# Optimization experiments

Hardware: AMD Instinct MI355X
Metric: run time of the kernel (lower is better)

Reference implementation:

```python
import jax, jax.numpy as jnp
import numpy as np

N = 100000      # num vertices
M = 100000      # num hyperedges
NNZ = 800000    # incidence pairs
IN_CH = 128
H, C = 8, 16    # heads, out_channels
NEG_SLOPE = 0.2


def setup_inputs() -> dict:
    key = jax.random.key(0)
    k1, k2, k3, k4, k5 = jax.random.split(key, 5)
    X = jax.random.normal(k1, (N, IN_CH), dtype=jnp.float32)
    vertex = jax.random.randint(k2, (NNZ,), 0, N, dtype=jnp.int32)
    edges = jax.random.randint(k3, (NNZ,), 0, M, dtype=jnp.int32)
    # glorot init: Linear W (in, H*C) and att_e (1, H, C)
    std_w = float(np.sqrt(6.0 / (IN_CH + H * C)))
    W = jax.random.uniform(k4, (IN_CH, H * C), minval=-std_w, maxval=std_w, dtype=jnp.float32)
    std_a = float(np.sqrt(6.0 / (H + C)))
    att_e = jax.random.uniform(k5, (1, H, C), minval=-std_a, maxval=std_a, dtype=jnp.float32)
    return {"X": X, "W": W, "att_e": att_e, "vertex": vertex, "edges": edges}


def reference(X, W, att_e, vertex, edges):
    Nn = X.shape[0]
    nnz = vertex.shape[0]
    # X0 = self.W(X)  -> (N, H*C), then view (N, H, C)
    X0 = X @ W
    Xh = X0.reshape(Nn, H, C)
    # gather per incidence, mean-aggregate to hyperedges (first_aggregate='mean')
    Xve = Xh[vertex]                                            # (nnz, H, C)
    e_sum = jax.ops.segment_sum(Xve, edges, num_segments=M)     # (M, H, C)
    e_cnt = jax.ops.segment_sum(jnp.ones((nnz,), X.dtype), edges, num_segments=M)
    Xe = e_sum / jnp.maximum(e_cnt, 1.0)[:, None, None]
    # edge attention logits
    alpha_e = (Xe * att_e).sum(-1)                              # (M, H)
    a = alpha_e[edges]                                          # (nnz, H)
    a = jnp.where(a >= 0, a, NEG_SLOPE * a)                     # leaky_relu
    # segment softmax over incidences grouped by destination vertex
    amax = jax.ops.segment_max(a, vertex, num_segments=Nn)      # (N, H)
    amax = jnp.where(jnp.isfinite(amax), amax, 0.0)
    ex = jnp.exp(a - amax[vertex])
    denom = jax.ops.segment_sum(ex, vertex, num_segments=Nn)
    alpha = ex / (denom[vertex] + 1e-16)                        # (nnz, H)
    # attention-weighted scatter-sum back to vertices
    Xev = Xe[edges] * alpha[:, :, None]                         # (nnz, H, C)
    Xv = jax.ops.segment_sum(Xev, vertex, num_segments=Nn)      # (N, H, C)
    return Xv.reshape(Nn, H * C)
```

## Files before the change

kernel.cpp:

```cpp
#include <hip/hip_runtime.h>
#include <hip/hip_bf16.h>

#define N_V   100000
#define N_E   100000
#define NNZ_C 800000
#define HC    128
#define H_    8
#define C_    16
#define NEG   0.2f
#define BSH   9
#define KPB   512
#define NBUCK 196
#define CAP   5120
#define CHUNK 4096
#define SCAT_NB ((NNZ_C + CHUNK - 1) / CHUNK)
#define GEMM_NB ((N_V + 63) / 64)

typedef __attribute__((ext_vector_type(8))) short bf16x8;
typedef __attribute__((ext_vector_type(4))) float f32x4;
typedef unsigned long long ull;

__device__ __forceinline__ short f2bf(float f) {
    unsigned u = __float_as_uint(f);
    unsigned r = (u + 0x7FFFu + ((u >> 16) & 1u)) >> 16;
    return (short)r;
}
__device__ __forceinline__ float bf2f(unsigned short u) {
    return __uint_as_float(((unsigned)u) << 16);
}
__device__ __forceinline__ unsigned pack2(float lo, float hi) {
    return ((unsigned)(unsigned short)f2bf(hi) << 16) | (unsigned short)f2bf(lo);
}
__device__ __forceinline__ void acc8w(float* acc, uint4 p, float wt) {
    acc[0] += __uint_as_float(p.x << 16) * wt;
    acc[1] += __uint_as_float(p.x & 0xFFFF0000u) * wt;
    acc[2] += __uint_as_float(p.y << 16) * wt;
    acc[3] += __uint_as_float(p.y & 0xFFFF0000u) * wt;
    acc[4] += __uint_as_float(p.z << 16) * wt;
    acc[5] += __uint_as_float(p.z & 0xFFFF0000u) * wt;
    acc[6] += __uint_as_float(p.w << 16) * wt;
    acc[7] += __uint_as_float(p.w & 0xFFFF0000u) * wt;
}
__device__ __forceinline__ void acc8(float* acc, uint4 p) {
    acc[0] += __uint_as_float(p.x << 16);
    acc[1] += __uint_as_float(p.x & 0xFFFF0000u);
    acc[2] += __uint_as_float(p.y << 16);
    acc[3] += __uint_as_float(p.y & 0xFFFF0000u);
    acc[4] += __uint_as_float(p.z << 16);
    acc[5] += __uint_as_float(p.z & 0xFFFF0000u);
    acc[6] += __uint_as_float(p.w << 16);
    acc[7] += __uint_as_float(p.w & 0xFFFF0000u);
}

__global__ __launch_bounds__(256) void wt_k(const float* __restrict__ W, unsigned short* __restrict__ Wf) {
    int i = blockIdx.x * 256 + threadIdx.x;
    int j    = i & 7;
    int lane = (i >> 3) & 63;
    int ct   = (i >> 9) & 7;
    int ks   = i >> 12;
    int kq = lane >> 4, cl = lane & 15;
    int k = 32 * ks + ((j < 4) ? (4 * kq + j) : (16 + 4 * kq + (j - 4)));
    int c = 16 * ct + cl;
    Wf[i] = (unsigned short)f2bf(W[k * 128 + c]);
}

__global__ __launch_bounds__(256) void fusedA_k(const float* __restrict__ X,
                                                const unsigned short* __restrict__ Wf,
                                                unsigned short* __restrict__ X0b,
                                                const int* __restrict__ edges,
                                                const int* __restrict__ vertex,
                                                int* __restrict__ bcur_e, int* __restrict__ bcur_v,
                                                unsigned* __restrict__ stage_e, unsigned* __restrict__ stage_v) {
    __shared__ int he[NBUCK], hv[NBUCK];
    int tid = threadIdx.x;

    if (blockIdx.x >= SCAT_NB) {
        int blk = blockIdx.x - SCAT_NB;
        int lane = tid & 63;
        int cl = lane & 15, kq = lane >> 4;
        int base = blk * 64 + (tid >> 6) * 16;
        int rowA = base + cl;
        int srcRow = (rowA < N_V) ? rowA : (N_V - 1);

        f32x4 acc[8] = {};
        const float4* X4 = (const float4*)X;
        const bf16x8* Wf8 = (const bf16x8*)Wf;

        #pragma unroll
        for (int ks = 0; ks < 4; ++ks) {
            float4 a0 = X4[(size_t)srcRow * 32 + 8 * ks + kq];
            float4 a1 = X4[(size_t)srcRow * 32 + 8 * ks + 4 + kq];
            bf16x8 af;
            af[0] = f2bf(a0.x); af[1] = f2bf(a0.y); af[2] = f2bf(a0.z); af[3] = f2bf(a0.w);
            af[4] = f2bf(a1.x); af[5] = f2bf(a1.y); af[6] = f2bf(a1.z); af[7] = f2bf(a1.w);
            #pragma unroll
            for (int ct = 0; ct < 8; ++ct) {
                bf16x8 bf = Wf8[((ks * 8 + ct) << 6) + lane];
                acc[ct] = __builtin_amdgcn_mfma_f32_16x16x32_bf16(af, bf, acc[ct], 0, 0, 0);
            }
        }
        int rbase = base + kq * 4;
        #pragma unroll
        for (int ct = 0; ct < 8; ++ct) {
            #pragma unroll
            for (int r = 0; r < 4; ++r) {
                int row = rbase + r;
                if (row < N_V) X0b[(size_t)row * 128 + ct * 16 + cl] = (unsigned short)f2bf(acc[ct][r]);
            }
        }
    } else {
        for (int i = tid; i < NBUCK; i += 256) { he[i] = 0; hv[i] = 0; }
        __syncthreads();
        int e0 = blockIdx.x * CHUNK;
        int e1 = e0 + CHUNK; if (e1 > NNZ_C) e1 = NNZ_C;
        for (int i = e0 + tid; i < e1; i += 256) {
            atomicAdd(&he[edges[i] >> BSH], 1);
            atomicAdd(&hv[vertex[i] >> BSH], 1);
        }
        __syncthreads();
        for (int i = tid; i < NBUCK; i += 256) {
            int c = he[i]; he[i] = c ? atomicAdd(&bcur_e[i], c) : 0;
            c = hv[i];     hv[i] = c ? atomicAdd(&bcur_v[i], c) : 0;
        }
        __syncthreads();
        for (int i = e0 + tid; i < e1; i += 256) {
            int ed = edges[i], v = vertex[i];
            int be = ed >> BSH, bv = v >> BSH;
            int pe = atomicAdd(&he[be], 1);
            stage_e[(size_t)be * CAP + pe] = ((unsigned)(ed & (KPB - 1)) << 17) | (unsigned)v;
            int pv = atomicAdd(&hv[bv], 1);
            stage_v[(size_t)bv * CAP + pv] = ((unsigned)(v & (KPB - 1)) << 17) | (unsigned)ed;
        }
    }
}

__global__ __launch_bounds__(512) void bsort_k(const unsigned* __restrict__ stage_e,
                                               const unsigned* __restrict__ stage_v,
                                               const int* __restrict__ bcur_e, const int* __restrict__ bcur_v,
                                               int* __restrict__ e_off, int* __restrict__ v_off,
                                               int* __restrict__ e_idx, int* __restrict__ v_idx) {
    bool isE = blockIdx.x < NBUCK;
    int b = isE ? blockIdx.x : blockIdx.x - NBUCK;
    const unsigned* stage = (isE ? stage_e : stage_v) + (size_t)b * CAP;
    const int* bcnt = isE ? bcur_e : bcur_v;
    int* off = isE ? e_off : v_off;
    int* idx = isE ? e_idx : v_idx;
    int t = threadIdx.x;

    __shared__ int sb[256];
    __shared__ int cntk[KPB];
    __shared__ int loc[KPB];
    if (t < 256) sb[t] = (t < NBUCK) ? bcnt[t] : 0;
    cntk[t] = 0;
    __syncthreads();
    for (int dd = 1; dd < 256; dd <<= 1) {
        int v = (t < 256 && t >= dd) ? sb[t - dd] : 0;
        __syncthreads();
        if (t < 256 && t >= dd) sb[t] += v;
        __syncthreads();
    }
    int cnt = bcnt[b];
    int bbase = sb[b] - cnt;

    for (int i = t; i < cnt; i += 512)
        atomicAdd(&cntk[stage[i] >> 17], 1);
    __syncthreads();
    int val = cntk[t];
    loc[t] = val;
    __syncthreads();
    for (int dd = 1; dd < 512; dd <<= 1) {
        int tv = (t >= dd) ? loc[t - dd] : 0;
        __syncthreads();
        loc[t] += tv;
        __syncthreads();
    }
    int pos0 = bbase + loc[t] - val;
    int key = (b << BSH) + t;
    if (key < N_V) off[key] = pos0;
    cntk[t] = pos0;
    __syncthreads();
    for (int i = t; i < cnt; i += 512) {
        unsigned p = stage[i];
        int pos = atomicAdd(&cntk[p >> 17], 1);
        idx[pos] = (int)(p & 0x1FFFF);
    }
    if (blockIdx.x == 0 && t == 0) { e_off[N_E] = NNZ_C; v_off[N_V] = NNZ_C; }
}

__global__ __launch_bounds__(256) void agg_gather_k(const uint4* __restrict__ X0b4,
                                                    const int* __restrict__ e_off,
                                                    const int* __restrict__ e_idx,
                                                    const float* __restrict__ att,
                                                    uint4* __restrict__ Xeb4,
                                                    float* __restrict__ alpha_l) {
    int wave = (int)((blockIdx.x * 256 + threadIdx.x) >> 6);
    int lane = threadIdx.x & 63;
    if (wave >= N_E) return;
    int beg = e_off[wave], end = e_off[wave + 1];
    int deg = end - beg;
    int j = lane & 15, g = lane >> 4;

    float acc[8] = {0.f, 0.f, 0.f, 0.f, 0.f, 0.f, 0.f, 0.f};
    const uint4 Z = {0u, 0u, 0u, 0u};

    if (deg <= 64) {
        int vl = (lane < deg) ? e_idx[beg + lane] : 0;
        for (int r0 = 0; r0 < deg; r0 += 16) {
            int r_0 = r0 + g, r_1 = r0 + 4 + g, r_2 = r0 + 8 + g, r_3 = r0 + 12 + g;
            int v_0 = __shfl(vl, r_0), v_1 = __shfl(vl, r_1);
            int v_2 = __shfl(vl, r_2), v_3 = __shfl(vl, r_3);
            uint4 p_0 = Z, p_1 = Z, p_2 = Z, p_3 = Z;
            if (r_0 < deg) p_0 = X0b4[(size_t)v_0 * 16 + j];
            if (r_1 < deg) p_1 = X0b4[(size_t)v_1 * 16 + j];
            if (r_2 < deg) p_2 = X0b4[(size_t)v_2 * 16 + j];
            if (r_3 < deg) p_3 = X0b4[(size_t)v_3 * 16 + j];
            acc8(acc, p_0); acc8(acc, p_1); acc8(acc, p_2); acc8(acc, p_3);
        }
    } else {
        for (int i0 = beg; i0 < end; i0 += 4) {
            int i = i0 + g;
            uint4 p = Z;
            if (i < end) p = X0b4[(size_t)e_idx[i] * 16 + j];
            acc8(acc, p);
        }
    }
    #pragma unroll
    for (int k = 0; k < 8; ++k) {
        acc[k] += __shfl_xor(acc[k], 16);
        acc[k] += __shfl_xor(acc[k], 32);
    }
    float inv = 1.f / fmaxf((float)deg, 1.f);
    uint4 o;
    o.x = pack2(acc[0] * inv, acc[1] * inv);
    o.y = pack2(acc[2] * inv, acc[3] * inv);
    o.z = pack2(acc[4] * inv, acc[5] * inv);
    o.w = pack2(acc[6] * inv, acc[7] * inv);
    if (g == 0) Xeb4[(size_t)wave * 16 + j] = o;

    const float4* att4 = (const float4*)att;
    float4 A0 = att4[2 * j], A1 = att4[2 * j + 1];
    float s = bf2f((unsigned short)(o.x & 0xFFFF)) * A0.x + bf2f((unsigned short)(o.x >> 16)) * A0.y
            + bf2f((unsigned short)(o.y & 0xFFFF)) * A0.z + bf2f((unsigned short)(o.y >> 16)) * A0.w
            + bf2f((unsigned short)(o.z & 0xFFFF)) * A1.x + bf2f((unsigned short)(o.z >> 16)) * A1.y
            + bf2f((unsigned short)(o.w & 0xFFFF)) * A1.z + bf2f((unsigned short)(o.w >> 16)) * A1.w;
    s += __shfl_xor(s, 1);
    if (g == 0 && (j & 1) == 0) {
        s = (s >= 0.f) ? s : NEG * s;
        alpha_l[wave * 8 + (j >> 1)] = s;
    }
}

__global__ __launch_bounds__(256) void out_fused_k(const uint4* __restrict__ Xeb4,
                                                   const float* __restrict__ alpha_l,
                                                   const int* __restrict__ v_off,
                                                   const int* __restrict__ v_idx,
                                                   float* __restrict__ out) {
    int wave = (int)((blockIdx.x * 256 + threadIdx.x) >> 6);
    int lane = threadIdx.x & 63;
    if (wave >= N_V) return;
    int beg = v_off[wave], end = v_off[wave + 1];
    int deg = end - beg;
    int j = lane & 15, g = lane >> 4, h = j >> 1;

    float acc[8] = {0.f, 0.f, 0.f, 0.f, 0.f, 0.f, 0.f, 0.f};
    float d = 0.f;
    const uint4 Z = {0u, 0u, 0u, 0u};

    if (deg <= 64) {
        int vl = (lane < deg) ? v_idx[beg + lane] : 0;
        for (int r0 = 0; r0 < deg; r0 += 16) {
            int r_0 = r0 + g, r_1 = r0 + 4 + g, r_2 = r0 + 8 + g, r_3 = r0 + 12 + g;
            int e_0 = __shfl(vl, r_0), e_1 = __shfl(vl, r_1);
            int e_2 = __shfl(vl, r_2), e_3 = __shfl(vl, r_3);
            bool b_0 = r_0 < deg, b_1 = r_1 < deg, b_2 = r_2 < deg, b_3 = r_3 < deg;
            float a_0 = 0.f, a_1 = 0.f, a_2 = 0.f, a_3 = 0.f;
            uint4 p_0 = Z, p_1 = Z, p_2 = Z, p_3 = Z;
            if (b_0) { a_0 = alpha_l[e_0 * 8 + h]; p_0 = Xeb4[(size_t)e_0 * 16 + j]; }
            if (b_1) { a_1 = alpha_l[e_1 * 8 + h]; p_1 = Xeb4[(size_t)e_1 * 16 + j]; }
            if (b_2) { a_2 = alpha_l[e_2 * 8 + h]; p_2 = Xeb4[(size_t)e_2 * 16 + j]; }
            if (b_3) { a_3 = alpha_l[e_3 * 8 + h]; p_3 = Xeb4[(size_t)e_3 * 16 + j]; }
            float w_0 = b_0 ? __expf(a_0) : 0.f;
            float w_1 = b_1 ? __expf(a_1) : 0.f;
            float w_2 = b_2 ? __expf(a_2) : 0.f;
            float w_3 = b_3 ? __expf(a_3) : 0.f;
            d += w_0 + w_1 + w_2 + w_3;
            acc8w(acc, p_0, w_0); acc8w(acc, p_1, w_1);
            acc8w(acc, p_2, w_2); acc8w(acc, p_3, w_3);
        }
    } else {
        for (int i0 = beg; i0 < end; i0 += 4) {
            int i = i0 + g;
            float w = 0.f;
            uint4 p = Z;
            if (i < end) {
                int ed = v_idx[i];
                w = __expf(alpha_l[ed * 8 + h]);
                p = Xeb4[(size_t)ed * 16 + j];
            }
            d += w;
            acc8w(acc, p, w);
        }
    }
    d += __shfl_xor(d, 16);
    d += __shfl_xor(d, 32);
    float rd = 1.f / (d + 1e-16f);
    #pragma unroll
    for (int k = 0; k < 8; ++k) {
        acc[k] += __shfl_xor(acc[k], 16);
        acc[k] += __shfl_xor(acc[k], 32);
        acc[k] *= rd;
    }
    if (g == 0) {
        float4* out4 = (float4*)out;
        float4 o0 = {acc[0], acc[1], acc[2], acc[3]};
        float4 o1 = {acc[4], acc[5], acc[6], acc[7]};
        out4[(size_t)wave * 32 + 2 * j]     = o0;
        out4[(size_t)wave * 32 + 2 * j + 1] = o1;
    }
}

extern "C" void kernel_launch(void* const* d_in, const int* in_sizes, int n_in,
                              void* d_out, int out_size, void* d_ws, size_t ws_size,
                              hipStream_t stream) {
    const float* X      = (const float*)d_in[0];
    const float* W      = (const float*)d_in[1];
    const float* att    = (const float*)d_in[2];
    const int*   vertex = (const int*)d_in[3];
    const int*   edges  = (const int*)d_in[4];
    float* out = (float*)d_out;

    unsigned short* X0b = (unsigned short*)d_ws;
    unsigned short* Xeb = X0b + (size_t)N_V * HC;
    unsigned* stage_e = (unsigned*)(Xeb + (size_t)N_E * HC);
    unsigned* stage_v = stage_e + (size_t)NBUCK * CAP;
    int*   e_off   = (int*)(stage_v + (size_t)NBUCK * CAP);
    int*   v_off   = e_off + (N_E + 1);
    int*   e_idx   = v_off + (N_V + 1);
    int*   v_idx   = e_idx + NNZ_C;
    float* alpha_l = (float*)(v_idx + NNZ_C);
    int*   bcur_e  = (int*)(alpha_l + (size_t)N_E * H_);
    int*   bcur_v  = bcur_e + NBUCK;
    unsigned short* Wf = (unsigned short*)(bcur_v + NBUCK);

    hipMemsetAsync(bcur_e, 0, sizeof(int) * 2 * NBUCK, stream);

    wt_k<<<64, 256, 0, stream>>>(W, Wf);

    fusedA_k<<<SCAT_NB + GEMM_NB, 256, 0, stream>>>(X, Wf, X0b, edges, vertex,
                                                    bcur_e, bcur_v, stage_e, stage_v);

    bsort_k<<<2 * NBUCK, 512, 0, stream>>>(stage_e, stage_v, bcur_e, bcur_v,
                                           e_off, v_off, e_idx, v_idx);

    agg_gather_k<<<(N_E * 64) / 256, 256, 0, stream>>>((const uint4*)X0b, e_off, e_idx, att,
                                                       (uint4*)Xeb, alpha_l);

    out_fused_k<<<(N_V * 64) / 256, 256, 0, stream>>>((const uint4*)Xeb, alpha_l, v_off, v_idx, out);
}
```

Baseline: 149.3 us.

## Process four segments per wave with 16 lanes each, precompute exp of edge logits

Both gather kernels now give each 16-lane quarter-wave its own hyperedge or vertex, instead of a whole wave per segment with a cross-lane reduction. That launches a quarter of the blocks and drops the shuffle reductions and idle lanes on small-degree segments. The edge kernel now stores exp(leaky_relu(logit)) so the output kernel skips the per-incidence exp. The costs are lower memory parallelism per segment and divergence between quarter-waves whose segments differ in degree. The exp is still taken without subtracting the max.

```diff
diff --git a/kernel.cpp b/kernel.cpp
--- a/kernel.cpp
+++ b/kernel.cpp
@@ -18,7 +18,6 @@
 
 typedef __attribute__((ext_vector_type(8))) short bf16x8;
 typedef __attribute__((ext_vector_type(4))) float f32x4;
-typedef unsigned long long ull;
 
 __device__ __forceinline__ short f2bf(float f) {
     unsigned u = __float_as_uint(f);
@@ -192,42 +191,33 @@
                                                     const int* __restrict__ e_idx,
                                                     const float* __restrict__ att,
                                                     uint4* __restrict__ Xeb4,
-                                                    float* __restrict__ alpha_l) {
-    int wave = (int)((blockIdx.x * 256 + threadIdx.x) >> 6);
+                                                    float* __restrict__ aexp) {
     int lane = threadIdx.x & 63;
-    if (wave >= N_E) return;
-    int beg = e_off[wave], end = e_off[wave + 1];
+    int s = lane >> 4, j = lane & 15;
+    int e = ((int)(blockIdx.x * 256 + threadIdx.x) >> 6) * 4 + s;
+    int beg = e_off[e], end = e_off[e + 1];
     int deg = end - beg;
-    int j = lane & 15, g = lane >> 4;
+    int sbase = s << 4;
 
     float acc[8] = {0.f, 0.f, 0.f, 0.f, 0.f, 0.f, 0.f, 0.f};
     const uint4 Z = {0u, 0u, 0u, 0u};
 
-    if (deg <= 64) {
-        int vl = (lane < deg) ? e_idx[beg + lane] : 0;
-        for (int r0 = 0; r0 < deg; r0 += 16) {
-            int r_0 = r0 + g, r_1 = r0 + 4 + g, r_2 = r0 + 8 + g, r_3 = r0 + 12 + g;
-            int v_0 = __shfl(vl, r_0), v_1 = __shfl(vl, r_1);
-            int v_2 = __shfl(vl, r_2), v_3 = __shfl(vl, r_3);
-            uint4 p_0 = Z, p_1 = Z, p_2 = Z, p_3 = Z;
-            if (r_0 < deg) p_0 = X0b4[(size_t)v_0 * 16 + j];
-            if (r_1 < deg) p_1 = X0b4[(size_t)v_1 * 16 + j];
-            if (r_2 < deg) p_2 = X0b4[(size_t)v_2 * 16 + j];
-            if (r_3 < deg) p_3 = X0b4[(size_t)v_3 * 16 + j];
+    for (int i0 = 0; i0 < deg; i0 += 16) {
+        int rem = deg - i0;
+        int myidx = (j < rem) ? e_idx[beg + i0 + j] : 0;
+        int lim = (rem < 16) ? rem : 16;
+        for (int t = 0; t < lim; t += 4) {
+            int v_0 = __shfl(myidx, sbase + t);
+            int v_1 = __shfl(myidx, sbase + ((t + 1) & 15));
+            int v_2 = __shfl(myidx, sbase + ((t + 2) & 15));
+            int v_3 = __shfl(myidx, sbase + ((t + 3) & 15));
+            bool c1 = (t + 1) < lim, c2 = (t + 2) < lim, c3 = (t + 3) < lim;
+            uint4 p_0 = X0b4[(size_t)v_0 * 16 + j];
+            uint4 p_1 = c1 ? X0b4[(size_t)v_1 * 16 + j] : Z;
+            uint4 p_2 = c2 ? X0b4[(size_t)v_2 * 16 + j] : Z;
+            uint4 p_3 = c3 ? X0b4[(size_t)v_3 * 16 + j] : Z;
             acc8(acc, p_0); acc8(acc, p_1); acc8(acc, p_2); acc8(acc, p_3);
         }
-    } else {
-        for (int i0 = beg; i0 < end; i0 += 4) {
-            int i = i0 + g;
-            uint4 p = Z;
-            if (i < end) p = X0b4[(size_t)e_idx[i] * 16 + j];
-            acc8(acc, p);
-        }
-    }
-    #pragma unroll
-    for (int k = 0; k < 8; ++k) {
-        acc[k] += __shfl_xor(acc[k], 16);
-        acc[k] += __shfl_xor(acc[k], 32);
     }
     float inv = 1.f / fmaxf((float)deg, 1.f);
     uint4 o;
@@ -235,88 +225,66 @@
     o.y = pack2(acc[2] * inv, acc[3] * inv);
     o.z = pack2(acc[4] * inv, acc[5] * inv);
     o.w = pack2(acc[6] * inv, acc[7] * inv);
-    if (g == 0) Xeb4[(size_t)wave * 16 + j] = o;
+    Xeb4[(size_t)e * 16 + j] = o;
 
     const float4* att4 = (const float4*)att;
     float4 A0 = att4[2 * j], A1 = att4[2 * j + 1];
-    float s = bf2f((unsigned short)(o.x & 0xFFFF)) * A0.x + bf2f((unsigned short)(o.x >> 16)) * A0.y
-            + bf2f((unsigned short)(o.y & 0xFFFF)) * A0.z + bf2f((unsigned short)(o.y >> 16)) * A0.w
-            + bf2f((unsigned short)(o.z & 0xFFFF)) * A1.x + bf2f((unsigned short)(o.z >> 16)) * A1.y
-            + bf2f((unsigned short)(o.w & 0xFFFF)) * A1.z + bf2f((unsigned short)(o.w >> 16)) * A1.w;
-    s += __shfl_xor(s, 1);
-    if (g == 0 && (j & 1) == 0) {
-        s = (s >= 0.f) ? s : NEG * s;
-        alpha_l[wave * 8 + (j >> 1)] = s;
+    float s2 = bf2f((unsigned short)(o.x & 0xFFFF)) * A0.x + bf2f((unsigned short)(o.x >> 16)) * A0.y
+             + bf2f((unsigned short)(o.y & 0xFFFF)) * A0.z + bf2f((unsigned short)(o.y >> 16)) * A0.w
+             + bf2f((unsigned short)(o.z & 0xFFFF)) * A1.x + bf2f((unsigned short)(o.z >> 16)) * A1.y
+             + bf2f((unsigned short)(o.w & 0xFFFF)) * A1.z + bf2f((unsigned short)(o.w >> 16)) * A1.w;
+    s2 += __shfl_xor(s2, 1);
+    if ((j & 1) == 0) {
+        s2 = (s2 >= 0.f) ? s2 : NEG * s2;
+        aexp[e * 8 + (j >> 1)] = __expf(s2);
     }
 }
 
 __global__ __launch_bounds__(256) void out_fused_k(const uint4* __restrict__ Xeb4,
-                                                   const float* __restrict__ alpha_l,
+                                                   const float* __restrict__ aexp,
                                                    const int* __restrict__ v_off,
                                                    const int* __restrict__ v_idx,
                                                    float* __restrict__ out) {
-    int wave = (int)((blockIdx.x * 256 + threadIdx.x) >> 6);
     int lane = threadIdx.x & 63;
-    if (wave >= N_V) return;
-    int beg = v_off[wave], end = v_off[wave + 1];
+    int s = lane >> 4, j = lane & 15, h = j >> 1;
+    int v = ((int)(blockIdx.x * 256 + threadIdx.x) >> 6) * 4 + s;
+    int beg = v_off[v], end = v_off[v + 1];
     int deg = end - beg;
-    int j = lane & 15, g = lane >> 4, h = j >> 1;
+    int sbase = s << 4;
 
     float acc[8] = {0.f, 0.f, 0.f, 0.f, 0.f, 0.f, 0.f, 0.f};
     float d = 0.f;
     const uint4 Z = {0u, 0u, 0u, 0u};
 
-    if (deg <= 64) {
-        int vl = (lane < deg) ? v_idx[beg + lane] : 0;
-        for (int r0 = 0; r0 < deg; r0 += 16) {
-            int r_0 = r0 + g, r_1 = r0 + 4 + g, r_2 = r0 + 8 + g, r_3 = r0 + 12 + g;
-            int e_0 = __shfl(vl, r_0), e_1 = __shfl(vl, r_1);
-            int e_2 = __shfl(vl, r_2), e_3 = __shfl(vl, r_3);
-            bool b_0 = r_0 < deg, b_1 = r_1 < deg, b_2 = r_2 < deg, b_3 = r_3 < deg;
-            float a_0 = 0.f, a_1 = 0.f, a_2 = 0.f, a_3 = 0.f;
-            uint4 p_0 = Z, p_1 = Z, p_2 = Z, p_3 = Z;
-            if (b_0) { a_0 = alpha_l[e_0 * 8 + h]; p_0 = Xeb4[(size_t)e_0 * 16 + j]; }
-            if (b_1) { a_1 = alpha_l[e_1 * 8 + h]; p_1 = Xeb4[(size_t)e_1 * 16 + j]; }
-            if (b_2) { a_2 = alpha_l[e_2 * 8 + h]; p_2 = Xeb4[(size_t)e_2 * 16 + j]; }
-            if (b_3) { a_3 = alpha_l[e_3 * 8 + h]; p_3 = Xeb4[(size_t)e_3 * 16 + j]; }
-            float w_0 = b_0 ? __expf(a_0) : 0.f;
-            float w_1 = b_1 ? __expf(a_1) : 0.f;
-            float w_2 = b_2 ? __expf(a_2) : 0.f;
-            float w_3 = b_3 ? __expf(a_3) : 0.f;
+    for (int i0 = 0; i0 < deg; i0 += 16) {
+        int rem = deg - i0;
+        int myidx = (j < rem) ? v_idx[beg + i0 + j] : 0;
+        int lim = (rem < 16) ? rem : 16;
+        for (int t = 0; t < lim; t += 4) {
+            int e_0 = __shfl(myidx, sbase + t);
+            int e_1 = __shfl(myidx, sbase + ((t + 1) & 15));
+            int e_2 = __shfl(myidx, sbase + ((t + 2) & 15));
+            int e_3 = __shfl(myidx, sbase + ((t + 3) & 15));
+            bool c1 = (t + 1) < lim, c2 = (t + 2) < lim, c3 = (t + 3) < lim;
+            float w_0 = aexp[e_0 * 8 + h];
+            float w_1 = c1 ? aexp[e_1 * 8 + h] : 0.f;
+            float w_2 = c2 ? aexp[e_2 * 8 + h] : 0.f;
+            float w_3 = c3 ? aexp[e_3 * 8 + h] : 0.f;
+            uint4 p_0 = Xeb4[(size_t)e_0 * 16 + j];
+            uint4 p_1 = c1 ? Xeb4[(size_t)e_1 * 16 + j] : Z;
+            uint4 p_2 = c2 ? Xeb4[(size_t)e_2 * 16 + j] : Z;
+            uint4 p_3 = c3 ? Xeb4[(size_t)e_3 * 16 + j] : Z;
             d += w_0 + w_1 + w_2 + w_3;
             acc8w(acc, p_0, w_0); acc8w(acc, p_1, w_1);
             acc8w(acc, p_2, w_2); acc8w(acc, p_3, w_3);
         }
-    } else {
-        for (int i0 = beg; i0 < end; i0 += 4) {
-            int i = i0 + g;
-            float w = 0.f;
-            uint4 p = Z;
-            if (i < end) {
-                int ed = v_idx[i];
-                w = __expf(alpha_l[ed * 8 + h]);
-                p = Xeb4[(size_t)ed * 16 + j];
-            }
-            d += w;
-            acc8w(acc, p, w);
-        }
-    }
-    d += __shfl_xor(d, 16);
-    d += __shfl_xor(d, 32);
+    }
     float rd = 1.f / (d + 1e-16f);
-    #pragma unroll
-    for (int k = 0; k < 8; ++k) {
-        acc[k] += __shfl_xor(acc[k], 16);
-        acc[k] += __shfl_xor(acc[k], 32);
-        acc[k] *= rd;
-    }
-    if (g == 0) {
-        float4* out4 = (float4*)out;
-        float4 o0 = {acc[0], acc[1], acc[2], acc[3]};
-        float4 o1 = {acc[4], acc[5], acc[6], acc[7]};
-        out4[(size_t)wave * 32 + 2 * j]     = o0;
-        out4[(size_t)wave * 32 + 2 * j + 1] = o1;
-    }
+    float4* out4 = (float4*)out;
+    float4 o0 = {acc[0] * rd, acc[1] * rd, acc[2] * rd, acc[3] * rd};
+    float4 o1 = {acc[4] * rd, acc[5] * rd, acc[6] * rd, acc[7] * rd};
+    out4[(size_t)v * 32 + 2 * j]     = o0;
+    out4[(size_t)v * 32 + 2 * j + 1] = o1;
 }
 
 extern "C" void kernel_launch(void* const* d_in, const int* in_sizes, int n_in,
@@ -337,8 +305,8 @@
     int*   v_off   = e_off + (N_E + 1);
     int*   e_idx   = v_off + (N_V + 1);
     int*   v_idx   = e_idx + NNZ_C;
-    float* alpha_l = (float*)(v_idx + NNZ_C);
-    int*   bcur_e  = (int*)(alpha_l + (size_t)N_E * H_);
+    float* aexp    = (float*)(v_idx + NNZ_C);
+    int*   bcur_e  = (int*)(aexp + (size_t)N_E * H_);
     int*   bcur_v  = bcur_e + NBUCK;
     unsigned short* Wf = (unsigned short*)(bcur_v + NBUCK);
 
@@ -352,8 +320,8 @@
     bsort_k<<<2 * NBUCK, 512, 0, stream>>>(stage_e, stage_v, bcur_e, bcur_v,
                                            e_off, v_off, e_idx, v_idx);
 
-    agg_gather_k<<<(N_E * 64) / 256, 256, 0, stream>>>((const uint4*)X0b, e_off, e_idx, att,
-                                                       (uint4*)Xeb, alpha_l);
-
-    out_fused_k<<<(N_V * 64) / 256, 256, 0, stream>>>((const uint4*)Xeb, alpha_l, v_off, v_idx, out);
-}
+    agg_gather_k<<<N_E / 16, 256, 0, stream>>>((const uint4*)X0b, e_off, e_idx, att,
+                                               (uint4*)Xeb, aexp);
+
+    out_fused_k<<<N_V / 16, 256, 0, stream>>>((const uint4*)Xeb, aexp, v_off, v_idx, out);
+}
```

Measured after the change: 152.6 us. 2.3% more time.

## Overlap vertex bucket sort with edge aggregation and drop memset launch

Applied to the files above, without the earlier changes.

Splits the combined bucket-sort kernel so the edge-side sort runs alone, then merges the vertex-side sort into the same launch as the edge gather/attention kernel, since neither depends on the other. The counter zeroing and sentinel offset writes move into the weight-prep kernel, removing the separate memset. This cuts launches and lets the vertex sort overlap with the gather, but the merged kernel now uses 512-thread blocks with sort shared memory, which may lower occupancy for the gather path.

```diff
diff --git a/kernel.cpp b/kernel.cpp
--- a/kernel.cpp
+++ b/kernel.cpp
@@ -18,7 +18,6 @@
 
 typedef __attribute__((ext_vector_type(8))) short bf16x8;
 typedef __attribute__((ext_vector_type(4))) float f32x4;
-typedef unsigned long long ull;
 
 __device__ __forceinline__ short f2bf(float f) {
     unsigned u = __float_as_uint(f);
@@ -52,8 +51,53 @@
     acc[7] += __uint_as_float(p.w & 0xFFFF0000u);
 }
 
-__global__ __launch_bounds__(256) void wt_k(const float* __restrict__ W, unsigned short* __restrict__ Wf) {
+__device__ __forceinline__ void bsort_body(const unsigned* __restrict__ stage,
+                                           const int* __restrict__ bcnt,
+                                           int* __restrict__ off, int* __restrict__ idx,
+                                           int b, int t, int* sb, int* cntk, int* loc) {
+    if (t < 256) sb[t] = (t < NBUCK) ? bcnt[t] : 0;
+    cntk[t] = 0;
+    __syncthreads();
+    for (int dd = 1; dd < 256; dd <<= 1) {
+        int v = (t < 256 && t >= dd) ? sb[t - dd] : 0;
+        __syncthreads();
+        if (t < 256 && t >= dd) sb[t] += v;
+        __syncthreads();
+    }
+    int cnt = bcnt[b];
+    int bbase = sb[b] - cnt;
+    const unsigned* st = stage + (size_t)b * CAP;
+
+    for (int i = t; i < cnt; i += 512)
+        atomicAdd(&cntk[st[i] >> 17], 1);
+    __syncthreads();
+    int val = cntk[t];
+    loc[t] = val;
+    __syncthreads();
+    for (int dd = 1; dd < 512; dd <<= 1) {
+        int tv = (t >= dd) ? loc[t - dd] : 0;
+        __syncthreads();
+        loc[t] += tv;
+        __syncthreads();
+    }
+    int pos0 = bbase + loc[t] - val;
+    int key = (b << BSH) + t;
+    if (key < N_V) off[key] = pos0;
+    cntk[t] = pos0;
+    __syncthreads();
+    for (int i = t; i < cnt; i += 512) {
+        unsigned p = st[i];
+        int pos = atomicAdd(&cntk[p >> 17], 1);
+        idx[pos] = (int)(p & 0x1FFFF);
+    }
+}
+
+__global__ __launch_bounds__(256) void wt_k(const float* __restrict__ W, unsigned short* __restrict__ Wf,
+                                            int* __restrict__ bcur, int* __restrict__ e_off,
+                                            int* __restrict__ v_off) {
     int i = blockIdx.x * 256 + threadIdx.x;
+    if (i < 2 * NBUCK) bcur[i] = 0;
+    if (i == 0) { e_off[N_E] = NNZ_C; v_off[N_V] = NNZ_C; }
     int j    = i & 7;
     int lane = (i >> 3) & 63;
     int ct   = (i >> 9) & 7;
@@ -134,68 +178,29 @@
     }
 }
 
-__global__ __launch_bounds__(512) void bsort_k(const unsigned* __restrict__ stage_e,
-                                               const unsigned* __restrict__ stage_v,
-                                               const int* __restrict__ bcur_e, const int* __restrict__ bcur_v,
-                                               int* __restrict__ e_off, int* __restrict__ v_off,
-                                               int* __restrict__ e_idx, int* __restrict__ v_idx) {
-    bool isE = blockIdx.x < NBUCK;
-    int b = isE ? blockIdx.x : blockIdx.x - NBUCK;
-    const unsigned* stage = (isE ? stage_e : stage_v) + (size_t)b * CAP;
-    const int* bcnt = isE ? bcur_e : bcur_v;
-    int* off = isE ? e_off : v_off;
-    int* idx = isE ? e_idx : v_idx;
-    int t = threadIdx.x;
-
-    __shared__ int sb[256];
-    __shared__ int cntk[KPB];
-    __shared__ int loc[KPB];
-    if (t < 256) sb[t] = (t < NBUCK) ? bcnt[t] : 0;
-    cntk[t] = 0;
-    __syncthreads();
-    for (int dd = 1; dd < 256; dd <<= 1) {
-        int v = (t < 256 && t >= dd) ? sb[t - dd] : 0;
-        __syncthreads();
-        if (t < 256 && t >= dd) sb[t] += v;
-        __syncthreads();
-    }
-    int cnt = bcnt[b];
-    int bbase = sb[b] - cnt;
-
-    for (int i = t; i < cnt; i += 512)
-        atomicAdd(&cntk[stage[i] >> 17], 1);
-    __syncthreads();
-    int val = cntk[t];
-    loc[t] = val;
-    __syncthreads();
-    for (int dd = 1; dd < 512; dd <<= 1) {
-        int tv = (t >= dd) ? loc[t - dd] : 0;
-        __syncthreads();
-        loc[t] += tv;
-        __syncthreads();
-    }
-    int pos0 = bbase + loc[t] - val;
-    int key = (b << BSH) + t;
-    if (key < N_V) off[key] = pos0;
-    cntk[t] = pos0;
-    __syncthreads();
-    for (int i = t; i < cnt; i += 512) {
-        unsigned p = stage[i];
-        int pos = atomicAdd(&cntk[p >> 17], 1);
-        idx[pos] = (int)(p & 0x1FFFF);
-    }
-    if (blockIdx.x == 0 && t == 0) { e_off[N_E] = NNZ_C; v_off[N_V] = NNZ_C; }
-}
-
-__global__ __launch_bounds__(256) void agg_gather_k(const uint4* __restrict__ X0b4,
-                                                    const int* __restrict__ e_off,
-                                                    const int* __restrict__ e_idx,
-                                                    const float* __restrict__ att,
-                                                    uint4* __restrict__ Xeb4,
-                                                    float* __restrict__ alpha_l) {
-    int wave = (int)((blockIdx.x * 256 + threadIdx.x) >> 6);
+__global__ __launch_bounds__(512) void bsort_e_k(const unsigned* __restrict__ stage_e,
+                                                 const int* __restrict__ bcur_e,
+                                                 int* __restrict__ e_off, int* __restrict__ e_idx) {
+    __shared__ int sb[256], cntk[KPB], loc[KPB];
+    bsort_body(stage_e, bcur_e, e_off, e_idx, blockIdx.x, threadIdx.x, sb, cntk, loc);
+}
+
+__global__ __launch_bounds__(512) void merged_k(const unsigned* __restrict__ stage_v,
+                                                const int* __restrict__ bcur_v,
+                                                int* __restrict__ v_off, int* __restrict__ v_idx,
+                                                const uint4* __restrict__ X0b4,
+                                                const int* __restrict__ e_off,
+                                                const int* __restrict__ e_idx,
+                                                const float* __restrict__ att,
+                                                uint4* __restrict__ Xeb4,
+                                                float* __restrict__ alpha_l) {
+    __shared__ int sb[256], cntk[KPB], loc[KPB];
+    if (blockIdx.x < NBUCK) {
+        bsort_body(stage_v, bcur_v, v_off, v_idx, blockIdx.x, threadIdx.x, sb, cntk, loc);
+        return;
+    }
+    int wave = ((int)blockIdx.x - NBUCK) * 8 + ((int)threadIdx.x >> 6);
     int lane = threadIdx.x & 63;
-    if (wave >= N_E) return;
     int beg = e_off[wave], end = e_off[wave + 1];
     int deg = end - beg;
     int j = lane & 15, g = lane >> 4;
@@ -342,18 +347,16 @@
     int*   bcur_v  = bcur_e + NBUCK;
     unsigned short* Wf = (unsigned short*)(bcur_v + NBUCK);
 
-    hipMemsetAsync(bcur_e, 0, sizeof(int) * 2 * NBUCK, stream);
-
-    wt_k<<<64, 256, 0, stream>>>(W, Wf);
+    wt_k<<<64, 256, 0, stream>>>(W, Wf, bcur_e, e_off, v_off);
 
     fusedA_k<<<SCAT_NB + GEMM_NB, 256, 0, stream>>>(X, Wf, X0b, edges, vertex,
                                                     bcur_e, bcur_v, stage_e, stage_v);
 
-    bsort_k<<<2 * NBUCK, 512, 0, stream>>>(stage_e, stage_v, bcur_e, bcur_v,
-                                           e_off, v_off, e_idx, v_idx);
-
-    agg_gather_k<<<(N_E * 64) / 256, 256, 0, stream>>>((const uint4*)X0b, e_off, e_idx, att,
-                                                       (uint4*)Xeb, alpha_l);
+    bsort_e_k<<<NBUCK, 512, 0, stream>>>(stage_e, bcur_e, e_off, e_idx);
+
+    merged_k<<<NBUCK + N_E / 8, 512, 0, stream>>>(stage_v, bcur_v, v_off, v_idx,
+                                                  (const uint4*)X0b, e_off, e_idx, att,
+                                                  (uint4*)Xeb, alpha_l);
 
     out_fused_k<<<(N_V * 64) / 256, 256, 0, stream>>>((const uint4*)Xeb, alpha_l, v_off, v_idx, out);
 }
```

Measured after the change: 142.0 us. -4.8%, faster.
